# Performance work log

Measured on AMD Instinct MI355X. Metric: run time of the kernel, lower is better.

## Reference

```python
import jax, jax.numpy as jnp
import numpy as np

N = 20000
NUM_CLASSES = 30


def setup_inputs() -> dict:
    key = jax.random.key(0)
    k1, k2, k3 = jax.random.split(key, 3)
    mean_3d = jax.random.normal(k1, (N, 3), dtype=jnp.float32)
    mean_3d_cano = jax.random.normal(k2, (N, 3), dtype=jnp.float32)
    segm_labels = jax.random.randint(k3, (N,), 0, NUM_CLASSES, dtype=jnp.int32)
    return {"mean_3d": mean_3d, "mean_3d_cano": mean_3d_cano, "segm_labels": segm_labels}


def reference(mean_3d, mean_3d_cano, segm_labels):
    # Brute-force K=1 nearest neighbor: squared euclidean distance
    # d2[i, j] = ||x_i||^2 - 2 x_i . y_j + ||y_j||^2  -> [N, N]
    x2 = jnp.sum(mean_3d * mean_3d, axis=-1, keepdims=True)          # [N, 1]
    y2 = jnp.sum(mean_3d_cano * mean_3d_cano, axis=-1)               # [N]
    d2 = x2 - 2.0 * (mean_3d @ mean_3d_cano.T) + y2[None, :]         # [N, N]
    nearest_ids = jnp.argmin(d2, axis=1)                              # [N]
    matched_labels = segm_labels[nearest_ids]
    semantic_inconsistent = (matched_labels != segm_labels)
    semantic_loss = semantic_inconsistent.astype(jnp.float32).mean()
    return semantic_loss
```

## Files before the change

kernel.cpp:

```cpp
#include <hip/hip_runtime.h>

#define N_PTS 20000
#define NA 20480
#define NB 20032
#define TILES_TOTAL 640
#define A_BYTES  (NA * 16 * 2)
#define B_BYTES  (NB * 16 * 2)
#define BEST_OFF (A_BYTES + B_BYTES)
#define CNT_OFF  (BEST_OFF + NB * 8)

typedef __attribute__((ext_vector_type(8))) short bf16x8;
typedef __attribute__((ext_vector_type(16))) float f32x16;

static __device__ __forceinline__ unsigned short f2bf(float f) {
    unsigned int u = __float_as_uint(f);
    unsigned int r = (u + 0x7FFFu + ((u >> 16) & 1u)) >> 16;
    return (unsigned short)r;
}
static __device__ __forceinline__ float bf2f(unsigned short h) {
    return __uint_as_float(((unsigned int)h) << 16);
}

static __device__ __forceinline__ unsigned long long packmin(float v, int idx) {
    unsigned u = __float_as_uint(v);
    u ^= (u & 0x80000000u) ? 0xFFFFFFFFu : 0x80000000u;
    return ((unsigned long long)u << 32) | (unsigned)idx;
}

__global__ __launch_bounds__(256) void nn_prep(const float* __restrict__ q,
                                               const float* __restrict__ c,
                                               unsigned short* __restrict__ Amat,
                                               unsigned short* __restrict__ Bmat,
                                               unsigned long long* __restrict__ best,
                                               unsigned int* __restrict__ counters) {
    const int m = blockIdx.x * 256 + (int)threadIdx.x;
    if (m < 2) counters[m] = 0u;
    if (m < NB) best[m] = 0xFFFFFFFFFFFFFFFFull;
    if (m < NA) {
        unsigned short a[16];
        #pragma unroll
        for (int r = 0; r < 16; ++r) a[r] = 0;
        if (m < N_PTS) {
            const float cx = c[m * 3 + 0], cy = c[m * 3 + 1], cz = c[m * 3 + 2];
            const unsigned short hx = f2bf(cx), hy = f2bf(cy), hz = f2bf(cz);
            const float lx = cx - bf2f(hx), ly = cy - bf2f(hy), lz = cz - bf2f(hz);
            const float y2 = fmaf(cx, cx, fmaf(cy, cy, cz * cz));
            const unsigned short y2h = f2bf(y2);
            const unsigned short y2l = f2bf(y2 - bf2f(y2h));
            a[0] = f2bf(-2.f * bf2f(hx)); a[1] = f2bf(-2.f * bf2f(hy)); a[2] = f2bf(-2.f * bf2f(hz));
            a[3] = a[0]; a[4] = a[1]; a[5] = a[2];
            a[6] = f2bf(-2.f * lx); a[7] = f2bf(-2.f * ly); a[8] = f2bf(-2.f * lz);
            a[9] = y2h; a[10] = y2l;
        } else {
            a[9] = f2bf(1e30f);
        }
        unsigned int* o = (unsigned int*)(Amat + (size_t)m * 16);
        #pragma unroll
        for (int r = 0; r < 8; ++r)
            o[r] = (unsigned int)a[2 * r] | ((unsigned int)a[2 * r + 1] << 16);
    }
    if (m < NB) {
        unsigned short b[16];
        #pragma unroll
        for (int r = 0; r < 16; ++r) b[r] = 0;
        if (m < N_PTS) {
            const float qx = q[m * 3 + 0], qy = q[m * 3 + 1], qz = q[m * 3 + 2];
            const unsigned short hx = f2bf(qx), hy = f2bf(qy), hz = f2bf(qz);
            b[0] = hx; b[1] = hy; b[2] = hz;
            b[3] = f2bf(qx - bf2f(hx)); b[4] = f2bf(qy - bf2f(hy)); b[5] = f2bf(qz - bf2f(hz));
            b[6] = hx; b[7] = hy; b[8] = hz;
            b[9] = f2bf(1.0f); b[10] = f2bf(1.0f);
        }
        unsigned int* o = (unsigned int*)(Bmat + (size_t)m * 16);
        #pragma unroll
        for (int r = 0; r < 8; ++r)
            o[r] = (unsigned int)b[2 * r] | ((unsigned int)b[2 * r + 1] << 16);
    }
}

static __device__ __forceinline__ float tree_min16(const f32x16& v) {
    const float t0 = fminf(fminf(v[0], v[1]), v[2]);
    const float t1 = fminf(fminf(v[3], v[4]), v[5]);
    const float t2 = fminf(fminf(v[6], v[7]), v[8]);
    const float t3 = fminf(fminf(v[9], v[10]), v[11]);
    const float t4 = fminf(fminf(v[12], v[13]), v[14]);
    const float t5 = fminf(fminf(t0, t1), v[15]);
    const float t6 = fminf(fminf(t2, t3), t4);
    return fminf(t5, t6);
}

static __device__ __forceinline__ int tile_argreg(const f32x16& v) {
    float pm = __uint_as_float(0x7F800000u);
    #pragma unroll
    for (int r = 0; r < 16; ++r)
        pm = fminf(pm, __uint_as_float((__float_as_uint(v[r]) & 0xFFFFFFF0u) | (unsigned)r));
    return (int)(__float_as_uint(pm) & 15u);
}

template<int LC>
__global__ __launch_bounds__(256) void nn_main(const unsigned short* __restrict__ Amat,
                                               const unsigned short* __restrict__ Bmat,
                                               unsigned long long* __restrict__ best) {
    constexpr int C = 1 << LC;
    constexpr int TPC = TILES_TOTAL >> LC;

    const int wav = (int)(threadIdx.x >> 6);
    const int ch = blockIdx.x & (C - 1);
    const int qg = ((int)blockIdx.x >> LC) * 4 + wav;
    if (qg >= 313) return;
    const int lane = (int)(threadIdx.x & 63);
    const int qbase = qg * 64;
    const int l31 = lane & 31;
    const int half = lane >> 5;

    const bf16x8 b1 = *(const bf16x8*)(Bmat + (size_t)(qbase + l31) * 16 + half * 8);
    const bf16x8 b2 = *(const bf16x8*)(Bmat + (size_t)(qbase + 32 + l31) * 16 + half * 8);

    const f32x16 zacc = {0.f, 0.f, 0.f, 0.f, 0.f, 0.f, 0.f, 0.f,
                         0.f, 0.f, 0.f, 0.f, 0.f, 0.f, 0.f, 0.f};

    float bv1 = __uint_as_float(0x7F800000u), bv2 = bv1;
    int bp1 = 0, bp2 = 0;

    const unsigned short* Abase = Amat + ((size_t)(ch * TPC) * 32 + l31) * 16 + half * 8;
    const unsigned short* Ap = Abase;
    #pragma unroll 2
    for (int t = 0; t < TPC; ++t) {
        const bf16x8 af = *(const bf16x8*)Ap;
        Ap += 512;
        const f32x16 a1 = __builtin_amdgcn_mfma_f32_32x32x16_bf16(af, b1, zacc, 0, 0, 0);
        const f32x16 a2 = __builtin_amdgcn_mfma_f32_32x32x16_bf16(af, b2, zacc, 0, 0, 0);
        const float m1 = tree_min16(a1);
        if (m1 < bv1) bp1 = t;
        bv1 = fminf(bv1, m1);
        const float m2 = tree_min16(a2);
        if (m2 < bv2) bp2 = t;
        bv2 = fminf(bv2, m2);
    }

    int bi1, bi2;
    {
        const bf16x8 e1 = *(const bf16x8*)(Abase + (size_t)bp1 * 512);
        const f32x16 r1 = __builtin_amdgcn_mfma_f32_32x32x16_bf16(e1, b1, zacc, 0, 0, 0);
        const int rg1 = tile_argreg(r1);
        bi1 = (ch * TPC + bp1) * 32 + (rg1 & 3) + 8 * (rg1 >> 2) + 4 * half;
        const bf16x8 e2 = *(const bf16x8*)(Abase + (size_t)bp2 * 512);
        const f32x16 r2 = __builtin_amdgcn_mfma_f32_32x32x16_bf16(e2, b2, zacc, 0, 0, 0);
        const int rg2 = tile_argreg(r2);
        bi2 = (ch * TPC + bp2) * 32 + (rg2 & 3) + 8 * (rg2 >> 2) + 4 * half;
    }

    const float ov1 = __shfl_xor(bv1, 32);
    const int oi1 = __shfl_xor(bi1, 32);
    if (ov1 < bv1 || (ov1 == bv1 && oi1 < bi1)) { bv1 = ov1; bi1 = oi1; }
    const float ov2 = __shfl_xor(bv2, 32);
    const int oi2 = __shfl_xor(bi2, 32);
    if (ov2 < bv2 || (ov2 == bv2 && oi2 < bi2)) { bv2 = ov2; bi2 = oi2; }

    if (lane < 32) {
        atomicMin(&best[qbase + l31],      packmin(bv1, bi1));
        atomicMin(&best[qbase + 32 + l31], packmin(bv2, bi2));
    }
}

__global__ __launch_bounds__(256) void nn_final(const unsigned long long* __restrict__ best,
                                                const int* __restrict__ labels,
                                                unsigned int* __restrict__ count,
                                                unsigned int* __restrict__ ticket,
                                                float* __restrict__ out) {
    const int i = blockIdx.x * 256 + (int)threadIdx.x;
    int mism = 0;
    if (i < N_PTS) {
        int bidx = (int)(unsigned)(best[i] & 0xFFFFFFFFull);
        bidx = (bidx < 0) ? 0 : ((bidx >= N_PTS) ? (N_PTS - 1) : bidx);
        mism = (labels[bidx] != labels[i]) ? 1 : 0;
    }
    const unsigned long long msk = __ballot(mism != 0);
    __shared__ unsigned int bsum;
    if (threadIdx.x == 0) bsum = 0;
    __syncthreads();
    if ((threadIdx.x & 63) == 0) atomicAdd(&bsum, (unsigned)__popcll(msk));
    __syncthreads();
    if (threadIdx.x == 0) {
        atomicAdd(count, bsum);
        __threadfence();
        const unsigned t = atomicAdd(ticket, 1u);
        if (t == gridDim.x - 1) {
            __threadfence();
            const unsigned total = atomicAdd(count, 0u);
            out[0] = (float)total / (float)N_PTS;
        }
    }
}

extern "C" void kernel_launch(void* const* d_in, const int* in_sizes, int n_in,
                              void* d_out, int out_size, void* d_ws, size_t ws_size,
                              hipStream_t stream) {
    const float* mean_3d      = (const float*)d_in[0];
    const float* mean_3d_cano = (const float*)d_in[1];
    const int*   segm_labels  = (const int*)d_in[2];
    float* out = (float*)d_out;

    unsigned short* Amat = (unsigned short*)d_ws;
    unsigned short* Bmat = (unsigned short*)((char*)d_ws + A_BYTES);
    unsigned long long* best = (unsigned long long*)((char*)d_ws + BEST_OFF);
    unsigned int* counters = (unsigned int*)((char*)d_ws + CNT_OFF);

    constexpr int lc = 5;
    constexpr int C = 1 << lc;

    nn_prep<<<NA / 256, 256, 0, stream>>>(mean_3d, mean_3d_cano, Amat, Bmat, best, counters);
    nn_main<lc><<<C * 79, 256, 0, stream>>>(Amat, Bmat, best);
    nn_final<<<(N_PTS + 255) / 256, 256, 0, stream>>>(best, segm_labels, counters, counters + 1, out);
}
```

Measured before the change: 37.58 us.

## Stage A chunks in LDS with tile-major layout and fuse final reduction

The prep kernel now writes A in a tile-major layout matching the MFMA operand order. Each main block copies its 20 KB chunk of A into LDS once with coalesced 16-byte loads, and its four waves then read tiles from LDS instead of global memory. The separate final kernel is removed: the last block to finish, chosen by an atomic ticket, counts label mismatches and writes the loss. This drops one kernel launch and repeated global A reads, but adds an LDS staging barrier and a serial tail in one block.

```diff
diff --git a/kernel.cpp b/kernel.cpp
--- a/kernel.cpp
+++ b/kernel.cpp
@@ -4,6 +4,10 @@
 #define NA 20480
 #define NB 20032
 #define TILES_TOTAL 640
+#define LCHUNK 5
+#define NCHUNK 32
+#define TPC (TILES_TOTAL / NCHUNK)
+#define CHUNK_BYTES (TPC * 1024)
 #define A_BYTES  (NA * 16 * 2)
 #define B_BYTES  (NB * 16 * 2)
 #define BEST_OFF (A_BYTES + B_BYTES)
@@ -54,10 +58,17 @@
         } else {
             a[9] = f2bf(1e30f);
         }
-        unsigned int* o = (unsigned int*)(Amat + (size_t)m * 16);
-        #pragma unroll
-        for (int r = 0; r < 8; ++r)
-            o[r] = (unsigned int)a[2 * r] | ((unsigned int)a[2 * r + 1] << 16);
+        const int tile = m >> 5, l31 = m & 31;
+        unsigned int* d0 = (unsigned int*)(Amat + (size_t)tile * 512 + l31 * 8);
+        unsigned int* d1 = (unsigned int*)(Amat + (size_t)tile * 512 + 256 + l31 * 8);
+        d0[0] = (unsigned)a[0] | ((unsigned)a[1] << 16);
+        d0[1] = (unsigned)a[2] | ((unsigned)a[3] << 16);
+        d0[2] = (unsigned)a[4] | ((unsigned)a[5] << 16);
+        d0[3] = (unsigned)a[6] | ((unsigned)a[7] << 16);
+        d1[0] = (unsigned)a[8] | ((unsigned)a[9] << 16);
+        d1[1] = (unsigned)a[10] | ((unsigned)a[11] << 16);
+        d1[2] = (unsigned)a[12] | ((unsigned)a[13] << 16);
+        d1[3] = (unsigned)a[14] | ((unsigned)a[15] << 16);
     }
     if (m < NB) {
         unsigned short b[16];
@@ -97,99 +108,102 @@
     return (int)(__float_as_uint(pm) & 15u);
 }
 
-template<int LC>
 __global__ __launch_bounds__(256) void nn_main(const unsigned short* __restrict__ Amat,
                                                const unsigned short* __restrict__ Bmat,
-                                               unsigned long long* __restrict__ best) {
-    constexpr int C = 1 << LC;
-    constexpr int TPC = TILES_TOTAL >> LC;
-
-    const int wav = (int)(threadIdx.x >> 6);
-    const int ch = blockIdx.x & (C - 1);
-    const int qg = ((int)blockIdx.x >> LC) * 4 + wav;
-    if (qg >= 313) return;
-    const int lane = (int)(threadIdx.x & 63);
-    const int qbase = qg * 64;
+                                               unsigned long long* __restrict__ best,
+                                               const int* __restrict__ labels,
+                                               unsigned int* __restrict__ ticket,
+                                               float* __restrict__ out) {
+    __shared__ __align__(16) unsigned short lds[TPC * 512];
+    __shared__ unsigned int bsum;
+    __shared__ int islast;
+
+    const int tid = (int)threadIdx.x;
+    const int wav = tid >> 6;
+    const int lane = tid & 63;
     const int l31 = lane & 31;
     const int half = lane >> 5;
-
-    const bf16x8 b1 = *(const bf16x8*)(Bmat + (size_t)(qbase + l31) * 16 + half * 8);
-    const bf16x8 b2 = *(const bf16x8*)(Bmat + (size_t)(qbase + 32 + l31) * 16 + half * 8);
-
-    const f32x16 zacc = {0.f, 0.f, 0.f, 0.f, 0.f, 0.f, 0.f, 0.f,
-                         0.f, 0.f, 0.f, 0.f, 0.f, 0.f, 0.f, 0.f};
-
-    float bv1 = __uint_as_float(0x7F800000u), bv2 = bv1;
-    int bp1 = 0, bp2 = 0;
-
-    const unsigned short* Abase = Amat + ((size_t)(ch * TPC) * 32 + l31) * 16 + half * 8;
-    const unsigned short* Ap = Abase;
-    #pragma unroll 2
-    for (int t = 0; t < TPC; ++t) {
-        const bf16x8 af = *(const bf16x8*)Ap;
-        Ap += 512;
-        const f32x16 a1 = __builtin_amdgcn_mfma_f32_32x32x16_bf16(af, b1, zacc, 0, 0, 0);
-        const f32x16 a2 = __builtin_amdgcn_mfma_f32_32x32x16_bf16(af, b2, zacc, 0, 0, 0);
-        const float m1 = tree_min16(a1);
-        if (m1 < bv1) bp1 = t;
-        bv1 = fminf(bv1, m1);
-        const float m2 = tree_min16(a2);
-        if (m2 < bv2) bp2 = t;
-        bv2 = fminf(bv2, m2);
-    }
-
-    int bi1, bi2;
+    const int ch = (int)blockIdx.x & (NCHUNK - 1);
+    const int qg = ((int)blockIdx.x >> LCHUNK) * 4 + wav;
+
     {
-        const bf16x8 e1 = *(const bf16x8*)(Abase + (size_t)bp1 * 512);
-        const f32x16 r1 = __builtin_amdgcn_mfma_f32_32x32x16_bf16(e1, b1, zacc, 0, 0, 0);
-        const int rg1 = tile_argreg(r1);
-        bi1 = (ch * TPC + bp1) * 32 + (rg1 & 3) + 8 * (rg1 >> 2) + 4 * half;
-        const bf16x8 e2 = *(const bf16x8*)(Abase + (size_t)bp2 * 512);
-        const f32x16 r2 = __builtin_amdgcn_mfma_f32_32x32x16_bf16(e2, b2, zacc, 0, 0, 0);
-        const int rg2 = tile_argreg(r2);
-        bi2 = (ch * TPC + bp2) * 32 + (rg2 & 3) + 8 * (rg2 >> 2) + 4 * half;
-    }
-
-    const float ov1 = __shfl_xor(bv1, 32);
-    const int oi1 = __shfl_xor(bi1, 32);
-    if (ov1 < bv1 || (ov1 == bv1 && oi1 < bi1)) { bv1 = ov1; bi1 = oi1; }
-    const float ov2 = __shfl_xor(bv2, 32);
-    const int oi2 = __shfl_xor(bi2, 32);
-    if (ov2 < bv2 || (ov2 == bv2 && oi2 < bi2)) { bv2 = ov2; bi2 = oi2; }
-
-    if (lane < 32) {
-        atomicMin(&best[qbase + l31],      packmin(bv1, bi1));
-        atomicMin(&best[qbase + 32 + l31], packmin(bv2, bi2));
-    }
-}
-
-__global__ __launch_bounds__(256) void nn_final(const unsigned long long* __restrict__ best,
-                                                const int* __restrict__ labels,
-                                                unsigned int* __restrict__ count,
-                                                unsigned int* __restrict__ ticket,
-                                                float* __restrict__ out) {
-    const int i = blockIdx.x * 256 + (int)threadIdx.x;
-    int mism = 0;
-    if (i < N_PTS) {
-        int bidx = (int)(unsigned)(best[i] & 0xFFFFFFFFull);
-        bidx = (bidx < 0) ? 0 : ((bidx >= N_PTS) ? (N_PTS - 1) : bidx);
-        mism = (labels[bidx] != labels[i]) ? 1 : 0;
-    }
-    const unsigned long long msk = __ballot(mism != 0);
-    __shared__ unsigned int bsum;
-    if (threadIdx.x == 0) bsum = 0;
+        const uint4* src = (const uint4*)((const char*)Amat + (size_t)ch * CHUNK_BYTES);
+        uint4* dst = (uint4*)lds;
+        #pragma unroll
+        for (int it = 0; it < 5; ++it)
+            dst[it * 256 + tid] = src[it * 256 + tid];
+    }
     __syncthreads();
-    if ((threadIdx.x & 63) == 0) atomicAdd(&bsum, (unsigned)__popcll(msk));
+
+    if (qg < 313) {
+        const int qbase = qg * 64;
+        const bf16x8 b1 = *(const bf16x8*)(Bmat + (size_t)(qbase + l31) * 16 + half * 8);
+        const bf16x8 b2 = *(const bf16x8*)(Bmat + (size_t)(qbase + 32 + l31) * 16 + half * 8);
+
+        const f32x16 zacc = {0.f, 0.f, 0.f, 0.f, 0.f, 0.f, 0.f, 0.f,
+                             0.f, 0.f, 0.f, 0.f, 0.f, 0.f, 0.f, 0.f};
+
+        float bv1 = __uint_as_float(0x7F800000u), bv2 = bv1;
+        int bp1 = 0, bp2 = 0;
+
+        #pragma unroll 2
+        for (int t = 0; t < TPC; ++t) {
+            const bf16x8 af = *(const bf16x8*)(lds + (size_t)t * 512 + lane * 8);
+            const f32x16 a1 = __builtin_amdgcn_mfma_f32_32x32x16_bf16(af, b1, zacc, 0, 0, 0);
+            const f32x16 a2 = __builtin_amdgcn_mfma_f32_32x32x16_bf16(af, b2, zacc, 0, 0, 0);
+            const float m1 = tree_min16(a1);
+            if (m1 < bv1) bp1 = t;
+            bv1 = fminf(bv1, m1);
+            const float m2 = tree_min16(a2);
+            if (m2 < bv2) bp2 = t;
+            bv2 = fminf(bv2, m2);
+        }
+
+        int bi1, bi2;
+        {
+            const bf16x8 e1 = *(const bf16x8*)(lds + (size_t)bp1 * 512 + lane * 8);
+            const f32x16 r1 = __builtin_amdgcn_mfma_f32_32x32x16_bf16(e1, b1, zacc, 0, 0, 0);
+            const int rg1 = tile_argreg(r1);
+            bi1 = (ch * TPC + bp1) * 32 + (rg1 & 3) + 8 * (rg1 >> 2) + 4 * half;
+            const bf16x8 e2 = *(const bf16x8*)(lds + (size_t)bp2 * 512 + lane * 8);
+            const f32x16 r2 = __builtin_amdgcn_mfma_f32_32x32x16_bf16(e2, b2, zacc, 0, 0, 0);
+            const int rg2 = tile_argreg(r2);
+            bi2 = (ch * TPC + bp2) * 32 + (rg2 & 3) + 8 * (rg2 >> 2) + 4 * half;
+        }
+
+        const float ov1 = __shfl_xor(bv1, 32);
+        const int oi1 = __shfl_xor(bi1, 32);
+        if (ov1 < bv1 || (ov1 == bv1 && oi1 < bi1)) { bv1 = ov1; bi1 = oi1; }
+        const float ov2 = __shfl_xor(bv2, 32);
+        const int oi2 = __shfl_xor(bi2, 32);
+        if (ov2 < bv2 || (ov2 == bv2 && oi2 < bi2)) { bv2 = ov2; bi2 = oi2; }
+
+        const unsigned long long pk = half ? packmin(bv2, bi2) : packmin(bv1, bi1);
+        atomicMin(&best[qbase + lane], pk);
+    }
+
     __syncthreads();
-    if (threadIdx.x == 0) {
-        atomicAdd(count, bsum);
+    if (tid == 0) {
         __threadfence();
-        const unsigned t = atomicAdd(ticket, 1u);
-        if (t == gridDim.x - 1) {
-            __threadfence();
-            const unsigned total = atomicAdd(count, 0u);
-            out[0] = (float)total / (float)N_PTS;
-        }
+        islast = (atomicAdd(ticket, 1u) == (unsigned)gridDim.x - 1u) ? 1 : 0;
+        bsum = 0u;
+    }
+    __syncthreads();
+
+    if (islast) {
+        unsigned cnt = 0;
+        for (int i = tid; i < N_PTS; i += 256) {
+            const unsigned long long b =
+                __hip_atomic_load(&best[i], __ATOMIC_RELAXED, __HIP_MEMORY_SCOPE_AGENT);
+            int bidx = (int)(unsigned)(b & 0xFFFFFFFFull);
+            bidx = (bidx < 0) ? 0 : ((bidx >= N_PTS) ? (N_PTS - 1) : bidx);
+            cnt += (labels[bidx] != labels[i]) ? 1u : 0u;
+        }
+        #pragma unroll
+        for (int off = 32; off > 0; off >>= 1) cnt += __shfl_down(cnt, off);
+        if ((tid & 63) == 0) atomicAdd(&bsum, cnt);
+        __syncthreads();
+        if (tid == 0) out[0] = (float)bsum / (float)N_PTS;
     }
 }
 
@@ -206,10 +220,6 @@
     unsigned long long* best = (unsigned long long*)((char*)d_ws + BEST_OFF);
     unsigned int* counters = (unsigned int*)((char*)d_ws + CNT_OFF);
 
-    constexpr int lc = 5;
-    constexpr int C = 1 << lc;
-
     nn_prep<<<NA / 256, 256, 0, stream>>>(mean_3d, mean_3d_cano, Amat, Bmat, best, counters);
-    nn_main<lc><<<C * 79, 256, 0, stream>>>(Amat, Bmat, best);
-    nn_final<<<(N_PTS + 255) / 256, 256, 0, stream>>>(best, segm_labels, counters, counters + 1, out);
-}
+    nn_main<<<NCHUNK * 79, 256, 0, stream>>>(Amat, Bmat, best, segm_labels, counters, out);
+}
```

Measured after the change: 91.05 us. +142.3%, slower.
